# Kernel tuning notes

Measured on AMD Instinct MI355X. Metric: run time of the kernel, lower is better.

The kernel has to match this reference:

```python
import jax, jax.numpy as jnp
import numpy as np

BS, H, L, D = 16, 16, 4096, 32  # bs, n_heads, seq_len(=q_len), head_dim

def setup_inputs() -> dict:
    key = jax.random.key(0)
    kq, kk, kv = jax.random.split(key, 3)
    q = jax.random.normal(kq, (BS, H, L, D), dtype=jnp.float32)
    k = jax.random.normal(kk, (BS, H, D, L), dtype=jnp.float32)
    v = jax.random.normal(kv, (BS, H, L, D), dtype=jnp.float32)
    return {"q": q, "k": k, "v": v}

def reference(q, k, v):
    # reordered attention: scores = (k @ v) / sqrt(seq_len) -> [bs,h,d_k,d_v]
    seq_len = v.shape[2]
    scores = jnp.einsum('bhds,bhse->bhde', k, v) / jnp.sqrt(jnp.float32(seq_len))
    # faithful to source: softmax over dim=0 (the batch dimension)
    attn_weights = jax.nn.softmax(scores, axis=0)
    # dropout p=0.0 -> identity
    # output = q @ weights -> [bs,h,q_len,d_v]
    output = jnp.einsum('bhld,bhde->bhle', q, attn_weights)
    return output, attn_weights
```

## Files before the change

### kernel.cpp

```cpp
#include <hip/hip_runtime.h>

#define BS 16
#define NH 16
#define LQ 4096
#define DH 32

constexpr size_t OUT_ELEMS = (size_t)BS * NH * LQ * DH;
constexpr int HDE = NH * DH * DH;

__device__ __forceinline__ void async_cp16(float* dst, const float* src) {
    __builtin_amdgcn_global_load_lds(
        (const __attribute__((address_space(1))) void*)src,
        (__attribute__((address_space(3))) void*)dst, 16, 0, 0);
}

__device__ __forceinline__ void fma4(float4& a, float s, const float4& v) {
    a.x = fmaf(s, v.x, a.x);
    a.y = fmaf(s, v.y, a.y);
    a.z = fmaf(s, v.z, a.z);
    a.w = fmaf(s, v.w, a.w);
}

template<int NCH>
__global__ __launch_bounds__(256, 4) void kv_partial(const float* __restrict__ k,
                                                     const float* __restrict__ v,
                                                     float* __restrict__ part) {
    __shared__ float lds[4608];
    const int tid = threadIdx.x;
    const int w   = tid >> 6;
    const int l   = tid & 63;
    const int nsplit = 64 / NCH;
    const int p  = blockIdx.x % nsplit;
    const int bh = blockIdx.x / nsplit;

    const int dg = l >> 3;
    const int eg = l & 7;
    const int d0 = dg << 2;
    const int e0 = eg << 2;

    const float* kb = k + (size_t)bh * DH * LQ;
    const float* vb = v + (size_t)bh * LQ * DH;
    float* kt = lds;
    float* vt = lds + 2048;

    const int j0 = w << 1, j1 = j0 + 1;
    const size_t ks0 = (size_t)((j0 << 2) + (l >> 4)) * LQ + (((l & 15) ^ j0) << 2);
    const size_t ks1 = (size_t)((j1 << 2) + (l >> 4)) * LQ + (((l & 15) ^ j1) << 2);
    const int vdst0 = (j0 << 8) + (l << 2);
    const int vdst1 = (j1 << 8) + (l << 2);

    float4 acc[4];
#pragma unroll
    for (int i = 0; i < 4; ++i) acc[i] = make_float4(0.f, 0.f, 0.f, 0.f);

#pragma unroll
    for (int c = 0; c < NCH; ++c) {
        const int s0 = (p * NCH + c) << 6;
        if (c > 0) __syncthreads();

        async_cp16(kt + (j0 << 8), kb + ks0 + s0);
        async_cp16(kt + (j1 << 8), kb + ks1 + s0);
        async_cp16(vt + (j0 << 8), vb + ((size_t)s0 << 5) + vdst0);
        async_cp16(vt + (j1 << 8), vb + ((size_t)s0 << 5) + vdst1);
        __syncthreads();

#pragma unroll
        for (int st = 0; st < 4; ++st) {
            const int cc = (w << 2) + st;
            const int ko = (cc ^ dg) << 2;
            float4 kq[4], vv[4];
#pragma unroll
            for (int i = 0; i < 4; ++i)
                kq[i] = *(const float4*)(kt + ((d0 + i) << 6) + ko);
#pragma unroll
            for (int u = 0; u < 4; ++u)
                vv[u] = *(const float4*)(vt + (((cc << 2) + u) << 5) + e0);
#pragma unroll
            for (int u = 0; u < 4; ++u) {
#pragma unroll
                for (int i = 0; i < 4; ++i) {
                    const float ks = (u == 0) ? kq[i].x
                                   : (u == 1) ? kq[i].y
                                   : (u == 2) ? kq[i].z : kq[i].w;
                    fma4(acc[i], ks, vv[u]);
                }
            }
        }
    }

    __syncthreads();
    float* dst = lds + ((w << 6) + l) * 17;
#pragma unroll
    for (int i = 0; i < 4; ++i) *(float4*)(dst + (i << 2)) = acc[i];
    __syncthreads();

    const int d   = tid >> 3;
    const int eg2 = tid & 7;
    const int twp = (((d >> 2)) << 3) | eg2;
    const int q   = (d & 3) << 2;
    float4 r = make_float4(0.f, 0.f, 0.f, 0.f);
#pragma unroll
    for (int ww = 0; ww < 4; ++ww) {
        const float4 t = *(const float4*)(lds + ((ww << 6) + twp) * 17 + q);
        r.x += t.x; r.y += t.y; r.z += t.z; r.w += t.w;
    }
    *(float4*)(part + ((size_t)p * (BS * NH) + bh) * 1024 + (tid << 2)) = r;
}

__global__ __launch_bounds__(256) void reduce_p(const float* __restrict__ part,
                                                float* __restrict__ wts, int nsp) {
    const int gidx = blockIdx.x * 256 + threadIdx.x;
    float s = 0.f;
#pragma unroll 8
    for (int pp = 0; pp < nsp; ++pp)
        s += part[((size_t)pp << 18) + gidx];
    wts[gidx] = s * (1.0f / 64.0f);
}

__global__ __launch_bounds__(256) void softmax_b(float* __restrict__ wts) {
    const int idx = blockIdx.x * 256 + threadIdx.x;

    float sc[BS];
#pragma unroll
    for (int b = 0; b < BS; ++b) sc[b] = wts[((size_t)b << 14) + idx];
    float m = sc[0];
#pragma unroll
    for (int b = 1; b < BS; ++b) m = fmaxf(m, sc[b]);
    float sum = 0.f;
#pragma unroll
    for (int b = 0; b < BS; ++b) { sc[b] = __expf(sc[b] - m); sum += sc[b]; }
    const float inv = 1.0f / sum;
#pragma unroll
    for (int b = 0; b < BS; ++b) wts[((size_t)b << 14) + idx] = sc[b] * inv;
}

__global__ __launch_bounds__(256, 2) void qw(const float* __restrict__ q,
                                             const float* __restrict__ wts,
                                             float* __restrict__ out) {
    __shared__ float qs[128 * 36];
    const int blk = blockIdx.x;
    const int bh  = blk >> 5;
    const int lt  = blk & 31;
    const int tid = threadIdx.x;

    const float* qbase = q + ((size_t)bh * LQ + lt * 128) * DH;

#pragma unroll
    for (int pp = 0; pp < 4; ++pp) {
        const int idx = pp * 256 + tid;
        const int row = idx >> 3;
        const int c4  = idx & 7;
        const float4 t = *(const float4*)(qbase + idx * 4);
        *(float4*)(qs + row * 36 + c4 * 4) = t;
    }

    const int lsub = tid >> 3;
    const int e0   = (tid & 7) << 2;

    const int b = bh >> 4, h = bh & 15;
    float4 Wf[32];
    const float* wbase = wts + ((size_t)b << 14) + ((size_t)h << 10) + e0;
#pragma unroll
    for (int d = 0; d < 32; ++d) Wf[d] = *(const float4*)(wbase + d * DH);

    __syncthreads();

    float* obase = out + ((size_t)bh * LQ + lt * 128) * DH;

#pragma unroll
    for (int r = 0; r < 4; ++r) {
        const int lr = lsub + r * 32;
        const float* qrow = qs + lr * 36;
        float4 acc = {0, 0, 0, 0};
#pragma unroll
        for (int d4 = 0; d4 < 32; d4 += 4) {
            const float4 qv = *(const float4*)(qrow + d4);
            fma4(acc, qv.x, Wf[d4 + 0]);
            fma4(acc, qv.y, Wf[d4 + 1]);
            fma4(acc, qv.z, Wf[d4 + 2]);
            fma4(acc, qv.w, Wf[d4 + 3]);
        }
        *(float4*)(obase + (size_t)lr * DH + e0) = acc;
    }
}

extern "C" void kernel_launch(void* const* d_in, const int* in_sizes, int n_in,
                              void* d_out, int out_size, void* d_ws, size_t ws_size,
                              hipStream_t stream) {
    const float* q = (const float*)d_in[0];
    const float* k = (const float*)d_in[1];
    const float* v = (const float*)d_in[2];
    float* out  = (float*)d_out;
    float* wts  = out + OUT_ELEMS;
    float* part = (float*)d_ws;

    const size_t need32 = (size_t)32 * 256 * 1024 * 4;
    int nsp;
    if (ws_size >= need32) {
        kv_partial<2><<<256 * 32, 256, 0, stream>>>(k, v, part);
        nsp = 32;
    } else {
        kv_partial<8><<<256 * 8, 256, 0, stream>>>(k, v, part);
        nsp = 8;
    }
    reduce_p<<<(BS * HDE) / 256, 256, 0, stream>>>(part, wts, nsp);
    softmax_b<<<HDE / 256, 256, 0, stream>>>(wts);
    qw<<<BS * NH * (LQ / 128), 256, 0, stream>>>(q, wts, out);
}
```

Measured before the change: 138.9 us.

## Rewrite kv_partial as single-wave blocks with register-staged loads and 4x8 tiles

Restructures the k·v partial-product kernel to use 64-thread single-wavefront blocks. Global loads are staged through registers into swizzled LDS in place of global_load_lds, and compiler scheduling barriers replace block-wide __syncthreads. Each lane now accumulates a 4x8 tile over half of the sequence window, and the two halves are combined with cross-lane shuffles instead of an LDS reduction. The aim is to remove barrier and LDS-reduction overhead and to raise per-thread reuse, at the cost of more registers per lane and less latency hiding per block.

```diff
diff --git a/kernel.cpp b/kernel.cpp
--- a/kernel.cpp
+++ b/kernel.cpp
@@ -7,12 +7,6 @@
 
 constexpr size_t OUT_ELEMS = (size_t)BS * NH * LQ * DH;
 constexpr int HDE = NH * DH * DH;
-
-__device__ __forceinline__ void async_cp16(float* dst, const float* src) {
-    __builtin_amdgcn_global_load_lds(
-        (const __attribute__((address_space(1))) void*)src,
-        (__attribute__((address_space(3))) void*)dst, 16, 0, 0);
-}
 
 __device__ __forceinline__ void fma4(float4& a, float s, const float4& v) {
     a.x = fmaf(s, v.x, a.x);
@@ -21,90 +15,100 @@
     a.w = fmaf(s, v.w, a.w);
 }
 
-template<int NCH>
-__global__ __launch_bounds__(256, 4) void kv_partial(const float* __restrict__ k,
-                                                     const float* __restrict__ v,
-                                                     float* __restrict__ part) {
-    __shared__ float lds[4608];
-    const int tid = threadIdx.x;
-    const int w   = tid >> 6;
-    const int l   = tid & 63;
-    const int nsplit = 64 / NCH;
+template<int NWIN>
+__global__ __launch_bounds__(64) void kv_partial(const float* __restrict__ k,
+                                                 const float* __restrict__ v,
+                                                 float* __restrict__ part) {
+    __shared__ float kt[1024];
+    __shared__ float vt[1024];
+    const int l  = threadIdx.x;
+    const int nsplit = 128 / NWIN;
     const int p  = blockIdx.x % nsplit;
     const int bh = blockIdx.x / nsplit;
 
-    const int dg = l >> 3;
-    const int eg = l & 7;
+    const int sp = l >> 5;
+    const int dg = (l >> 2) & 7;
+    const int eg = l & 3;
     const int d0 = dg << 2;
-    const int e0 = eg << 2;
+    const int e0 = eg << 3;
 
     const float* kb = k + (size_t)bh * DH * LQ;
     const float* vb = v + (size_t)bh * LQ * DH;
-    float* kt = lds;
-    float* vt = lds + 2048;
-
-    const int j0 = w << 1, j1 = j0 + 1;
-    const size_t ks0 = (size_t)((j0 << 2) + (l >> 4)) * LQ + (((l & 15) ^ j0) << 2);
-    const size_t ks1 = (size_t)((j1 << 2) + (l >> 4)) * LQ + (((l & 15) ^ j1) << 2);
-    const int vdst0 = (j0 << 8) + (l << 2);
-    const int vdst1 = (j1 << 8) + (l << 2);
-
-    float4 acc[4];
-#pragma unroll
-    for (int i = 0; i < 4; ++i) acc[i] = make_float4(0.f, 0.f, 0.f, 0.f);
-
-#pragma unroll
-    for (int c = 0; c < NCH; ++c) {
-        const int s0 = (p * NCH + c) << 6;
-        if (c > 0) __syncthreads();
-
-        async_cp16(kt + (j0 << 8), kb + ks0 + s0);
-        async_cp16(kt + (j1 << 8), kb + ks1 + s0);
-        async_cp16(vt + (j0 << 8), vb + ((size_t)s0 << 5) + vdst0);
-        async_cp16(vt + (j1 << 8), vb + ((size_t)s0 << 5) + vdst1);
-        __syncthreads();
+
+    const int krow8 = l >> 3;
+    const int kcs   = l & 7;
+    const int ksw   = l >> 5;
+
+    float4 acc[4][2];
+#pragma unroll
+    for (int i = 0; i < 4; ++i) {
+        acc[i][0] = make_float4(0.f, 0.f, 0.f, 0.f);
+        acc[i][1] = make_float4(0.f, 0.f, 0.f, 0.f);
+    }
+
+#pragma unroll
+    for (int c = 0; c < NWIN; ++c) {
+        const int wb = (p * NWIN + c) << 5;
+
+        float4 kst[4], vst[4];
+#pragma unroll
+        for (int j = 0; j < 4; ++j) {
+            const int r    = (j << 3) + krow8;
+            const int csrc = kcs ^ (((j << 1) + ksw) & 7);
+            kst[j] = *(const float4*)(kb + (size_t)r * LQ + wb + (csrc << 2));
+        }
+#pragma unroll
+        for (int j = 0; j < 4; ++j) {
+            const int s = (j << 3) + krow8;
+            vst[j] = *(const float4*)(vb + ((size_t)(wb + s) << 5) + (kcs << 2));
+        }
+#pragma unroll
+        for (int j = 0; j < 4; ++j) *(float4*)(kt + (j << 8) + (l << 2)) = kst[j];
+#pragma unroll
+        for (int j = 0; j < 4; ++j) *(float4*)(vt + (j << 8) + (l << 2)) = vst[j];
+        __builtin_amdgcn_sched_barrier(0);
 
 #pragma unroll
         for (int st = 0; st < 4; ++st) {
-            const int cc = (w << 2) + st;
-            const int ko = (cc ^ dg) << 2;
-            float4 kq[4], vv[4];
+            const int cc = (sp << 2) + st;
+            float4 kq[4];
 #pragma unroll
             for (int i = 0; i < 4; ++i)
-                kq[i] = *(const float4*)(kt + ((d0 + i) << 6) + ko);
-#pragma unroll
-            for (int u = 0; u < 4; ++u)
-                vv[u] = *(const float4*)(vt + (((cc << 2) + u) << 5) + e0);
+                kq[i] = *(const float4*)(kt + ((d0 + i) << 5) + (((cc ^ dg) & 7) << 2));
 #pragma unroll
             for (int u = 0; u < 4; ++u) {
+                const int s = (cc << 2) + u;
+                const float4 vu0 = *(const float4*)(vt + (s << 5) + e0);
+                const float4 vu1 = *(const float4*)(vt + (s << 5) + e0 + 4);
 #pragma unroll
                 for (int i = 0; i < 4; ++i) {
                     const float ks = (u == 0) ? kq[i].x
                                    : (u == 1) ? kq[i].y
                                    : (u == 2) ? kq[i].z : kq[i].w;
-                    fma4(acc[i], ks, vv[u]);
+                    fma4(acc[i][0], ks, vu0);
+                    fma4(acc[i][1], ks, vu1);
                 }
             }
         }
-    }
-
-    __syncthreads();
-    float* dst = lds + ((w << 6) + l) * 17;
-#pragma unroll
-    for (int i = 0; i < 4; ++i) *(float4*)(dst + (i << 2)) = acc[i];
-    __syncthreads();
-
-    const int d   = tid >> 3;
-    const int eg2 = tid & 7;
-    const int twp = (((d >> 2)) << 3) | eg2;
-    const int q   = (d & 3) << 2;
-    float4 r = make_float4(0.f, 0.f, 0.f, 0.f);
-#pragma unroll
-    for (int ww = 0; ww < 4; ++ww) {
-        const float4 t = *(const float4*)(lds + ((ww << 6) + twp) * 17 + q);
-        r.x += t.x; r.y += t.y; r.z += t.z; r.w += t.w;
-    }
-    *(float4*)(part + ((size_t)p * (BS * NH) + bh) * 1024 + (tid << 2)) = r;
+        __builtin_amdgcn_sched_barrier(0);
+    }
+
+#pragma unroll
+    for (int i = 0; i < 4; ++i)
+#pragma unroll
+        for (int h = 0; h < 2; ++h) {
+            acc[i][h].x += __shfl_xor(acc[i][h].x, 32);
+            acc[i][h].y += __shfl_xor(acc[i][h].y, 32);
+            acc[i][h].z += __shfl_xor(acc[i][h].z, 32);
+            acc[i][h].w += __shfl_xor(acc[i][h].w, 32);
+        }
+
+    float* pb = part + ((size_t)p << 18) + ((size_t)bh << 10);
+#pragma unroll
+    for (int i = 0; i < 4; ++i) {
+        const float4 wv = (sp == 0) ? acc[i][0] : acc[i][1];
+        *(float4*)(pb + ((d0 + i) << 5) + e0 + (sp << 2)) = wv;
+    }
 }
 
 __global__ __launch_bounds__(256) void reduce_p(const float* __restrict__ part,
@@ -197,10 +201,10 @@
     const size_t need32 = (size_t)32 * 256 * 1024 * 4;
     int nsp;
     if (ws_size >= need32) {
-        kv_partial<2><<<256 * 32, 256, 0, stream>>>(k, v, part);
+        kv_partial<4><<<256 * 32, 64, 0, stream>>>(k, v, part);
         nsp = 32;
     } else {
-        kv_partial<8><<<256 * 8, 256, 0, stream>>>(k, v, part);
+        kv_partial<16><<<256 * 8, 64, 0, stream>>>(k, v, part);
         nsp = 8;
     }
     reduce_p<<<(BS * HDE) / 256, 256, 0, stream>>>(part, wts, nsp);
```

Result: no change. 141.1 us (+1.6%).
